# Performance work log

Measured on AMD Instinct MI355X. Metric: run time of the kernel, lower is better.

## Reference

```python
import jax, jax.numpy as jnp
import numpy as np


def _graph_conv(x, src, dst, W_rel, b_rel, W_root):
    # PyG GraphConv (aggr='add'): out = lin_rel(sum_{j->i} x_j) + lin_root(x_i)
    agg = jax.ops.segment_sum(x[src], dst, num_segments=x.shape[0])  # [N, d]
    return agg @ W_rel + b_rel + x @ W_root


def setup_inputs() -> dict:
    N, E, D, H, G = 50000, 800000, 128, 128, 256
    key = jax.random.key(0)
    ks = jax.random.split(key, 24)
    x = jax.random.normal(ks[0], (N, D), dtype=jnp.float32)
    edge_index = jax.random.randint(ks[1], (2, E), 0, N, dtype=jnp.int64)
    batch = jnp.sort(jax.random.randint(ks[2], (N,), 0, G, dtype=jnp.int64))
    inp = {"x": x, "edge_index": edge_index, "batch": batch, "num_graphs": G}
    dims = [(D, H), (H, H), (H, H), (H, H), (H, H)]
    for i, (din, dout) in enumerate(dims, 1):
        s = 1.0 / np.sqrt(din)
        inp[f"W_rel{i}"] = jax.random.normal(ks[3 * i], (din, dout), dtype=jnp.float32) * s
        inp[f"b_rel{i}"] = jax.random.normal(ks[3 * i + 1], (dout,), dtype=jnp.float32) * s
        inp[f"W_root{i}"] = jax.random.normal(ks[3 * i + 2], (din, dout), dtype=jnp.float32) * s
    inp["fc1_W"] = jax.random.normal(ks[18], (H, H), dtype=jnp.float32) / np.sqrt(H)
    inp["fc1_b"] = jax.random.normal(ks[19], (H,), dtype=jnp.float32) / np.sqrt(H)
    inp["fc2_W"] = jax.random.normal(ks[20], (H, 1), dtype=jnp.float32) / np.sqrt(H)
    inp["fc2_b"] = jax.random.normal(ks[21], (1,), dtype=jnp.float32) / np.sqrt(H)
    return inp


def reference(x, edge_index, batch, num_graphs,
              W_rel1, b_rel1, W_root1,
              W_rel2, b_rel2, W_root2,
              W_rel3, b_rel3, W_root3,
              W_rel4, b_rel4, W_root4,
              W_rel5, b_rel5, W_root5,
              fc1_W, fc1_b, fc2_W, fc2_b):
    src, dst = edge_index[0], edge_index[1]
    h = x
    for Wr, br, Wl in ((W_rel1, b_rel1, W_root1), (W_rel2, b_rel2, W_root2),
                       (W_rel3, b_rel3, W_root3), (W_rel4, b_rel4, W_root4),
                       (W_rel5, b_rel5, W_root5)):
        h = jax.nn.relu(_graph_conv(h, src, dst, Wr, br, Wl))
    # global_add_pool -> [num_graphs, H]
    g = jax.ops.segment_sum(h, batch, num_segments=num_graphs)
    g = jax.nn.relu(g @ fc1_W + fc1_b)
    # dropout is identity in eval mode
    return g @ fc2_W + fc2_b  # [num_graphs, 1]
```

## Files before the change

### kernel.cpp

```cpp
#include <hip/hip_runtime.h>
#include <hip/hip_bf16.h>

typedef __attribute__((ext_vector_type(4))) float f32x4;
typedef __attribute__((ext_vector_type(8))) _Float16 f16x8;
typedef __attribute__((ext_vector_type(4))) _Float16 f16x4;

#define CHUNK 4096
#define BSH 7
#define CAP 4096

static __device__ __forceinline__ float2 h2f2(unsigned v) {
  _Float16 lo = __builtin_bit_cast(_Float16, (unsigned short)(v & 0xffffu));
  _Float16 hi = __builtin_bit_cast(_Float16, (unsigned short)(v >> 16));
  return make_float2((float)lo, (float)hi);
}
static __device__ __forceinline__ unsigned f2h2(float x, float y) {
  unsigned short lo = __builtin_bit_cast(unsigned short, (_Float16)x);
  unsigned short hi = __builtin_bit_cast(unsigned short, (_Float16)y);
  return ((unsigned)hi << 16) | lo;
}

__global__ __launch_bounds__(256) void cvt_kernel(const float* __restrict__ x,
                                                  _Float16* __restrict__ h, int total4) {
  int i = blockIdx.x * blockDim.x + threadIdx.x;
  if (i < total4) {
    float4 v = *(const float4*)(x + (size_t)i * 4);
    f16x4 o = {(_Float16)v.x, (_Float16)v.y, (_Float16)v.z, (_Float16)v.w};
    *(f16x4*)(h + (size_t)i * 4) = o;
  }
}

__global__ __launch_bounds__(256) void bhist_kernel(const int* __restrict__ dst,
                                                    int* __restrict__ gcnt, int E, int nb) {
  __shared__ int l[512];
  int t = threadIdx.x;
  for (int i = t; i < 512; i += 256) l[i] = 0;
  __syncthreads();
  int cbase = blockIdx.x * CHUNK;
  #pragma unroll
  for (int i = 0; i < CHUNK / 256; ++i) {
    int idx = cbase + i * 256 + t;
    if (idx < E) atomicAdd(&l[dst[idx] >> BSH], 1);
  }
  __syncthreads();
  for (int i = t; i < nb; i += 256) {
    int c = l[i];
    if (c) atomicAdd(&gcnt[i], c);
  }
}

__global__ __launch_bounds__(512) void bscan_kernel(const int* __restrict__ gcnt,
                                                    int* __restrict__ base,
                                                    int* __restrict__ gcursor, int nb, int E) {
  __shared__ int wsum[8], wpre[8];
  int t = threadIdx.x, lane = t & 63, w = t >> 6;
  int v = (t < nb) ? gcnt[t] : 0;
  int incl = v;
  #pragma unroll
  for (int o = 1; o < 64; o <<= 1) {
    int x = __shfl_up(incl, o, 64);
    if (lane >= o) incl += x;
  }
  if (lane == 63) wsum[w] = incl;
  __syncthreads();
  if (t == 0) {
    int run = 0;
    #pragma unroll
    for (int q = 0; q < 8; ++q) { wpre[q] = run; run += wsum[q]; }
  }
  __syncthreads();
  int excl = wpre[w] + incl - v;
  if (t < nb) { base[t] = excl; gcursor[t] = excl; }
  if (t == 0) base[nb] = E;
}

__global__ __launch_bounds__(256) void bscatter_kernel(const int* __restrict__ src,
                                                       const int* __restrict__ dst,
                                                       int* __restrict__ gcursor,
                                                       int2* __restrict__ pairs, int E, int nb) {
  __shared__ int lcnt[512], lstart[512], lpos[512], lgbase[512];
  __shared__ int2 lp[CHUNK];
  __shared__ int wsum[4], wpre[4];
  int t = threadIdx.x, lane = t & 63, w = t >> 6;
  for (int i = t; i < 512; i += 256) lcnt[i] = 0;
  __syncthreads();
  int cbase = blockIdx.x * CHUNK;
  int m = E - cbase; if (m > CHUNK) m = CHUNK;
  #pragma unroll
  for (int i = 0; i < CHUNK / 256; ++i) {
    int idx = i * 256 + t;
    if (idx < m) atomicAdd(&lcnt[dst[cbase + idx] >> BSH], 1);
  }
  __syncthreads();
  int c0 = lcnt[2 * t], c1 = lcnt[2 * t + 1];
  int s = c0 + c1, incl = s;
  #pragma unroll
  for (int o = 1; o < 64; o <<= 1) {
    int x = __shfl_up(incl, o, 64);
    if (lane >= o) incl += x;
  }
  if (lane == 63) wsum[w] = incl;
  __syncthreads();
  if (t == 0) {
    int run = 0;
    #pragma unroll
    for (int q = 0; q < 4; ++q) { wpre[q] = run; run += wsum[q]; }
  }
  __syncthreads();
  int excl = wpre[w] + incl - s;
  lstart[2 * t] = excl;         lpos[2 * t] = excl;
  lstart[2 * t + 1] = excl + c0; lpos[2 * t + 1] = excl + c0;
  if (2 * t < nb && c0 > 0) lgbase[2 * t] = atomicAdd(&gcursor[2 * t], c0);
  if (2 * t + 1 < nb && c1 > 0) lgbase[2 * t + 1] = atomicAdd(&gcursor[2 * t + 1], c1);
  __syncthreads();
  #pragma unroll
  for (int i = 0; i < CHUNK / 256; ++i) {
    int idx = i * 256 + t;
    if (idx < m) {
      int d = dst[cbase + idx], sv = src[cbase + idx];
      int p = atomicAdd(&lpos[d >> BSH], 1);
      lp[p] = make_int2(sv, d);
    }
  }
  __syncthreads();
  for (int i = t; i < m; i += 256) {
    int2 pr = lp[i];
    int b = pr.y >> BSH;
    pairs[lgbase[b] + (i - lstart[b])] = pr;
  }
}

__global__ __launch_bounds__(256) void bbuild_kernel(const int2* __restrict__ pairs,
                                                     const int* __restrict__ base,
                                                     int* __restrict__ row_ptr,
                                                     int* __restrict__ col, int N, int E) {
  __shared__ int cnt[128], cur[128], w2[2];
  __shared__ int cl[CAP];
  int b = blockIdx.x, t = threadIdx.x;
  int mb = base[b], me = base[b + 1], m = me - mb;
  if (t < 128) cnt[t] = 0;
  __syncthreads();
  for (int i = t; i < m; i += 256) atomicAdd(&cnt[pairs[mb + i].y & 127], 1);
  __syncthreads();
  int v = 0, incl = 0;
  if (t < 128) {
    v = cnt[t]; incl = v;
    #pragma unroll
    for (int o = 1; o < 64; o <<= 1) {
      int x = __shfl_up(incl, o, 64);
      if ((t & 63) >= o) incl += x;
    }
    if ((t & 63) == 63) w2[t >> 6] = incl;
  }
  __syncthreads();
  if (t < 128) {
    int excl = incl - v + ((t & 64) ? w2[0] : 0);
    cur[t] = excl;
    int node = (b << BSH) + t;
    if (node < N) row_ptr[node] = mb + excl;
  }
  if (b == 0 && t == 0) row_ptr[N] = E;
  __syncthreads();
  if (m <= CAP) {
    for (int i = t; i < m; i += 256) {
      int2 p = pairs[mb + i];
      int pos = atomicAdd(&cur[p.y & 127], 1);
      cl[pos] = p.x;
    }
    __syncthreads();
    for (int i = t; i < m; i += 256) col[mb + i] = cl[i];
  } else {
    for (int i = t; i < m; i += 256) {
      int2 p = pairs[mb + i];
      int pos = atomicAdd(&cur[p.y & 127], 1);
      col[mb + pos] = p.x;
    }
  }
}

__global__ void prep_kernel(const float* __restrict__ Wrel, const float* __restrict__ Wroot,
                            _Float16* __restrict__ Whi, _Float16* __restrict__ Wlo,
                            float wscale) {
  int idx = blockIdx.x * blockDim.x + threadIdx.x;
  int col = idx >> 8;
  int k = idx & 255;
  float v = (k < 128) ? Wrel[k * 128 + col] : Wroot[(k - 128) * 128 + col];
  v *= wscale;
  _Float16 hi = (_Float16)v;
  _Float16 lo = (_Float16)(v - (float)hi);
  Whi[idx] = hi;
  Wlo[idx] = lo;
}

__global__ __launch_bounds__(256) void gemm_fused(const _Float16* __restrict__ hin,
                                                  const int* __restrict__ row_ptr,
                                                  const int* __restrict__ col,
                                                  const _Float16* __restrict__ Whi,
                                                  const _Float16* __restrict__ Wlo,
                                                  const float* __restrict__ bias,
                                                  float bscale,
                                                  _Float16* __restrict__ out, int N) {
  __shared__ unsigned lds[64 * 64];
  const unsigned* __restrict__ h2 = (const unsigned*)hin;
  int t = threadIdx.x, w = t >> 6, lane = t & 63;
  int row_base = blockIdx.x * 64;

  for (int rr = 0; rr < 16; ++rr) {
    int row = row_base + w * 16 + rr;
    float ax = 0.f, ay = 0.f;
    if (row < N) {
      int s = __builtin_amdgcn_readfirstlane(row_ptr[row]);
      int e = __builtin_amdgcn_readfirstlane(row_ptr[row + 1]);
      int i = s;
      for (; i + 7 < e; i += 8) {
        unsigned v0 = h2[(size_t)col[i + 0] * 64 + lane];
        unsigned v1 = h2[(size_t)col[i + 1] * 64 + lane];
        unsigned v2 = h2[(size_t)col[i + 2] * 64 + lane];
        unsigned v3 = h2[(size_t)col[i + 3] * 64 + lane];
        unsigned v4 = h2[(size_t)col[i + 4] * 64 + lane];
        unsigned v5 = h2[(size_t)col[i + 5] * 64 + lane];
        unsigned v6 = h2[(size_t)col[i + 6] * 64 + lane];
        unsigned v7 = h2[(size_t)col[i + 7] * 64 + lane];
        float2 f0 = h2f2(v0), f1 = h2f2(v1), f2 = h2f2(v2), f3 = h2f2(v3);
        float2 f4 = h2f2(v4), f5 = h2f2(v5), f6 = h2f2(v6), f7 = h2f2(v7);
        ax += (f0.x + f1.x) + (f2.x + f3.x) + ((f4.x + f5.x) + (f6.x + f7.x));
        ay += (f0.y + f1.y) + (f2.y + f3.y) + ((f4.y + f5.y) + (f6.y + f7.y));
      }
      for (; i < e; ++i) {
        float2 f0 = h2f2(h2[(size_t)col[i] * 64 + lane]);
        ax += f0.x; ay += f0.y;
      }
    }
    int rl = w * 16 + rr;
    unsigned byte = (unsigned)(rl * 256 + lane * 4) ^ (unsigned)((rl & 7) << 4);
    lds[byte >> 2] = f2h2(ax, ay);
  }
  __syncthreads();

  int wv = w;
  int l16 = lane & 15;
  int khalf = lane >> 4;
  int koff = khalf * 8;
  int col_base = wv * 32;

  f32x4 acc[4][2];
  #pragma unroll
  for (int r = 0; r < 4; r++)
    #pragma unroll
    for (int c = 0; c < 2; c++) acc[r][c] = (f32x4){0.f, 0.f, 0.f, 0.f};

  #pragma unroll
  for (int ks = 0; ks < 8; ++ks) {
    int k0 = ks * 32;
    f16x8 bh[2], bl[2];
    #pragma unroll
    for (int c = 0; c < 2; c++) {
      int cc = col_base + c * 16 + l16;
      bh[c] = *(const f16x8*)(Whi + cc * 256 + k0 + koff);
      bl[c] = *(const f16x8*)(Wlo + cc * 256 + k0 + koff);
    }
    #pragma unroll
    for (int r = 0; r < 4; r++) {
      f16x8 a;
      if (ks < 4) {
        int arow = r * 16 + l16;
        unsigned byte = (unsigned)(arow * 256 + (k0 + koff) * 2) ^ (unsigned)((arow & 7) << 4);
        a = *(const f16x8*)((const char*)lds + byte);
      } else {
        int row = row_base + r * 16 + l16;
        if (row >= N) row = N - 1;
        a = *(const f16x8*)(hin + (size_t)row * 128 + (k0 - 128) + koff);
      }
      #pragma unroll
      for (int c = 0; c < 2; c++) {
        acc[r][c] = __builtin_amdgcn_mfma_f32_16x16x32_f16(a, bh[c], acc[r][c], 0, 0, 0);
        acc[r][c] = __builtin_amdgcn_mfma_f32_16x16x32_f16(a, bl[c], acc[r][c], 0, 0, 0);
      }
    }
  }

  #pragma unroll
  for (int r = 0; r < 4; r++) {
    #pragma unroll
    for (int c = 0; c < 2; c++) {
      int cc = col_base + c * 16 + l16;
      float b = bias[cc] * bscale;
      #pragma unroll
      for (int tt = 0; tt < 4; tt++) {
        int row = row_base + r * 16 + khalf * 4 + tt;
        if (row < N) {
          float v = acc[r][c][tt] + b;
          out[(size_t)row * 128 + cc] = (_Float16)(v > 0.f ? v : 0.f);
        }
      }
    }
  }
}

static __device__ __forceinline__ int lbound(const int* __restrict__ a, int n, int v) {
  int lo = 0, hi = n;
  while (lo < hi) {
    int m = (lo + hi) >> 1;
    if (a[m] < v) lo = m + 1; else hi = m;
  }
  return lo;
}

__global__ __launch_bounds__(128) void poolhead_kernel(const _Float16* __restrict__ h,
                                                       const int* __restrict__ batch,
                                                       const float* __restrict__ fc1W,
                                                       const float* __restrict__ fc1b,
                                                       const float* __restrict__ fc2W,
                                                       const float* __restrict__ fc2b,
                                                       float* __restrict__ out, int N,
                                                       float unscale) {
  int gid = blockIdx.x, j = threadIdx.x;
  int start = lbound(batch, N, gid);
  int end = lbound(batch, N, gid + 1);
  float acc = 0.f;
  int r = start;
  for (; r + 3 < end; r += 4) {
    acc += (float)h[(size_t)r * 128 + j] + (float)h[(size_t)(r + 1) * 128 + j] +
           (float)h[(size_t)(r + 2) * 128 + j] + (float)h[(size_t)(r + 3) * 128 + j];
  }
  for (; r < end; ++r) acc += (float)h[(size_t)r * 128 + j];
  __shared__ float grow[128];
  __shared__ float red[128];
  grow[j] = acc * unscale;
  __syncthreads();
  float a1 = fc1b[j];
  #pragma unroll 8
  for (int k = 0; k < 128; ++k) a1 = fmaf(grow[k], fc1W[k * 128 + j], a1);
  a1 = a1 > 0.f ? a1 : 0.f;
  red[j] = a1 * fc2W[j];
  __syncthreads();
  #pragma unroll
  for (int s2 = 64; s2 > 0; s2 >>= 1) {
    if (j < s2) red[j] += red[j + s2];
    __syncthreads();
  }
  if (j == 0) out[gid] = red[0] + fc2b[0];
}

extern "C" void kernel_launch(void* const* d_in, const int* in_sizes, int n_in,
                              void* d_out, int out_size, void* d_ws, size_t ws_size,
                              hipStream_t stream) {
  const float* x = (const float*)d_in[0];
  const int* edge = (const int*)d_in[1];
  const int* batch = (const int*)d_in[2];
  const int N = in_sizes[0] / 128;
  const int E = in_sizes[1] / 2;
  const int G = out_size;
  const int* esrc = edge;
  const int* edst = edge + E;
  const int NB = (N + 127) >> BSH;

  char* ws = (char*)d_ws;
  size_t off = 0;
  auto alloc = [&](size_t bytes) -> void* {
    void* p = ws + off;
    off = (off + bytes + 255) & ~(size_t)255;
    return p;
  };
  _Float16* x16  = (_Float16*)alloc((size_t)N * 128 * 2);
  _Float16* bufA = (_Float16*)alloc((size_t)N * 128 * 2);
  _Float16* bufB = (_Float16*)alloc((size_t)N * 128 * 2);
  _Float16* Whi  = (_Float16*)alloc((size_t)5 * 32768 * 2);
  _Float16* Wlo  = (_Float16*)alloc((size_t)5 * 32768 * 2);
  int* row_ptr   = (int*)alloc((size_t)(N + 1) * 4);
  int* col       = (int*)alloc((size_t)E * 4);
  int2* pairs    = (int2*)alloc((size_t)E * 8);
  int* gcnt      = (int*)alloc(512 * 4);
  int* base      = (int*)alloc(520 * 4);
  int* gcursor   = (int*)alloc(512 * 4);
  if (off > ws_size) return;

  hipMemsetAsync(gcnt, 0, 512 * 4, stream);

  int nb1 = (E + CHUNK - 1) / CHUNK;
  bhist_kernel<<<nb1, 256, 0, stream>>>(edst, gcnt, E, NB);
  bscan_kernel<<<1, 512, 0, stream>>>(gcnt, base, gcursor, NB, E);
  bscatter_kernel<<<nb1, 256, 0, stream>>>(esrc, edst, gcursor, pairs, E, NB);
  bbuild_kernel<<<NB, 256, 0, stream>>>(pairs, base, row_ptr, col, N, E);

  cvt_kernel<<<(N * 128 / 4 + 255) / 256, 256, 0, stream>>>(x, x16, N * 128 / 4);

  const float S = 8.0f;
  float bscale = 1.0f;
  for (int l = 0; l < 5; ++l) {
    prep_kernel<<<128, 256, 0, stream>>>((const float*)d_in[4 + 3 * l],
                                         (const float*)d_in[6 + 3 * l],
                                         Whi + (size_t)l * 32768, Wlo + (size_t)l * 32768,
                                         1.0f / S);
  }

  const _Float16* hin = x16;
  _Float16* hout = bufA;
  int gemm_grid = (N + 63) / 64;
  for (int l = 0; l < 5; ++l) {
    bscale /= S;
    gemm_fused<<<gemm_grid, 256, 0, stream>>>(hin, row_ptr, col,
                                              Whi + (size_t)l * 32768, Wlo + (size_t)l * 32768,
                                              (const float*)d_in[5 + 3 * l], bscale, hout, N);
    hin = hout;
    hout = (hout == bufA) ? bufB : bufA;
  }
  poolhead_kernel<<<G, 128, 0, stream>>>(hin, batch,
                                         (const float*)d_in[19], (const float*)d_in[20],
                                         (const float*)d_in[21], (const float*)d_in[22],
                                         (float*)d_out, N, 32768.0f);
}
```

Measured before the change: 421.6 us.

## Gather 16-byte vectors with four rows per wave and halve GEMM tile to 32 rows

The aggregation loop now gives each 16-lane group its own destination row and has each lane load 8 halves (16 bytes) per neighbor, so a wave handles four rows at once instead of one row with 4-byte loads. The block tile shrinks from 64 to 32 rows, doubling the grid and halving the MFMA accumulators per wave. This targets latency-bound gathers with narrow loads and serial per-row processing. The cost is that row_ptr loads are no longer wave-uniform, lanes in a wave can diverge on unequal degrees, and each W fragment is now loaded for fewer rows.

After: 408.8 us. -3.0%, faster.

```diff
diff --git a/kernel.cpp b/kernel.cpp
--- a/kernel.cpp
+++ b/kernel.cpp
@@ -8,12 +8,8 @@
 #define CHUNK 4096
 #define BSH 7
 #define CAP 4096
-
-static __device__ __forceinline__ float2 h2f2(unsigned v) {
-  _Float16 lo = __builtin_bit_cast(_Float16, (unsigned short)(v & 0xffffu));
-  _Float16 hi = __builtin_bit_cast(_Float16, (unsigned short)(v >> 16));
-  return make_float2((float)lo, (float)hi);
-}
+#define TM 32
+
 static __device__ __forceinline__ unsigned f2h2(float x, float y) {
   unsigned short lo = __builtin_bit_cast(unsigned short, (_Float16)x);
   unsigned short hi = __builtin_bit_cast(unsigned short, (_Float16)y);
@@ -108,7 +104,7 @@
   }
   __syncthreads();
   int excl = wpre[w] + incl - s;
-  lstart[2 * t] = excl;         lpos[2 * t] = excl;
+  lstart[2 * t] = excl;          lpos[2 * t] = excl;
   lstart[2 * t + 1] = excl + c0; lpos[2 * t + 1] = excl + c0;
   if (2 * t < nb && c0 > 0) lgbase[2 * t] = atomicAdd(&gcursor[2 * t], c0);
   if (2 * t + 1 < nb && c1 > 0) lgbase[2 * t + 1] = atomicAdd(&gcursor[2 * t + 1], c1);
@@ -200,52 +196,53 @@
                                                   const float* __restrict__ bias,
                                                   float bscale,
                                                   _Float16* __restrict__ out, int N) {
-  __shared__ unsigned lds[64 * 64];
-  const unsigned* __restrict__ h2 = (const unsigned*)hin;
+  __shared__ unsigned lds[TM * 64];
+  const f16x8* __restrict__ hp = (const f16x8*)hin;
   int t = threadIdx.x, w = t >> 6, lane = t & 63;
-  int row_base = blockIdx.x * 64;
-
-  for (int rr = 0; rr < 16; ++rr) {
-    int row = row_base + w * 16 + rr;
-    float ax = 0.f, ay = 0.f;
+  int g = lane >> 4, l16 = lane & 15;
+  int row_base = blockIdx.x * TM;
+
+  #pragma unroll
+  for (int chunk = 0; chunk < 2; ++chunk) {
+    int rl = w * 8 + chunk * 4 + g;
+    int row = row_base + rl;
+    float acc[8];
+    #pragma unroll
+    for (int q = 0; q < 8; ++q) acc[q] = 0.f;
     if (row < N) {
-      int s = __builtin_amdgcn_readfirstlane(row_ptr[row]);
-      int e = __builtin_amdgcn_readfirstlane(row_ptr[row + 1]);
+      int s = row_ptr[row], e = row_ptr[row + 1];
       int i = s;
-      for (; i + 7 < e; i += 8) {
-        unsigned v0 = h2[(size_t)col[i + 0] * 64 + lane];
-        unsigned v1 = h2[(size_t)col[i + 1] * 64 + lane];
-        unsigned v2 = h2[(size_t)col[i + 2] * 64 + lane];
-        unsigned v3 = h2[(size_t)col[i + 3] * 64 + lane];
-        unsigned v4 = h2[(size_t)col[i + 4] * 64 + lane];
-        unsigned v5 = h2[(size_t)col[i + 5] * 64 + lane];
-        unsigned v6 = h2[(size_t)col[i + 6] * 64 + lane];
-        unsigned v7 = h2[(size_t)col[i + 7] * 64 + lane];
-        float2 f0 = h2f2(v0), f1 = h2f2(v1), f2 = h2f2(v2), f3 = h2f2(v3);
-        float2 f4 = h2f2(v4), f5 = h2f2(v5), f6 = h2f2(v6), f7 = h2f2(v7);
-        ax += (f0.x + f1.x) + (f2.x + f3.x) + ((f4.x + f5.x) + (f6.x + f7.x));
-        ay += (f0.y + f1.y) + (f2.y + f3.y) + ((f4.y + f5.y) + (f6.y + f7.y));
+      for (; i + 3 < e; i += 4) {
+        int c0 = col[i], c1 = col[i + 1], c2 = col[i + 2], c3 = col[i + 3];
+        f16x8 v0 = hp[(size_t)c0 * 16 + l16];
+        f16x8 v1 = hp[(size_t)c1 * 16 + l16];
+        f16x8 v2 = hp[(size_t)c2 * 16 + l16];
+        f16x8 v3 = hp[(size_t)c3 * 16 + l16];
+        #pragma unroll
+        for (int q = 0; q < 8; ++q)
+          acc[q] += ((float)v0[q] + (float)v1[q]) + ((float)v2[q] + (float)v3[q]);
       }
       for (; i < e; ++i) {
-        float2 f0 = h2f2(h2[(size_t)col[i] * 64 + lane]);
-        ax += f0.x; ay += f0.y;
+        f16x8 v0 = hp[(size_t)col[i] * 16 + l16];
+        #pragma unroll
+        for (int q = 0; q < 8; ++q) acc[q] += (float)v0[q];
       }
     }
-    int rl = w * 16 + rr;
-    unsigned byte = (unsigned)(rl * 256 + lane * 4) ^ (unsigned)((rl & 7) << 4);
-    lds[byte >> 2] = f2h2(ax, ay);
-  }
-  __syncthreads();
-
-  int wv = w;
-  int l16 = lane & 15;
+    f16x8 o;
+    #pragma unroll
+    for (int q = 0; q < 8; ++q) o[q] = (_Float16)acc[q];
+    unsigned byte = (unsigned)(rl * 256 + l16 * 16) ^ (unsigned)((rl & 7) << 4);
+    *(f16x8*)((char*)lds + byte) = o;
+  }
+  __syncthreads();
+
   int khalf = lane >> 4;
   int koff = khalf * 8;
-  int col_base = wv * 32;
-
-  f32x4 acc[4][2];
-  #pragma unroll
-  for (int r = 0; r < 4; r++)
+  int col_base = w * 32;
+
+  f32x4 acc[2][2];
+  #pragma unroll
+  for (int r = 0; r < 2; r++)
     #pragma unroll
     for (int c = 0; c < 2; c++) acc[r][c] = (f32x4){0.f, 0.f, 0.f, 0.f};
 
@@ -260,11 +257,11 @@
       bl[c] = *(const f16x8*)(Wlo + cc * 256 + k0 + koff);
     }
     #pragma unroll
-    for (int r = 0; r < 4; r++) {
+    for (int r = 0; r < 2; r++) {
       f16x8 a;
       if (ks < 4) {
         int arow = r * 16 + l16;
-        unsigned byte = (unsigned)(arow * 256 + (k0 + koff) * 2) ^ (unsigned)((arow & 7) << 4);
+        unsigned byte = (unsigned)(arow * 256 + k0 * 2 + khalf * 16) ^ (unsigned)((arow & 7) << 4);
         a = *(const f16x8*)((const char*)lds + byte);
       } else {
         int row = row_base + r * 16 + l16;
@@ -280,7 +277,7 @@
   }
 
   #pragma unroll
-  for (int r = 0; r < 4; r++) {
+  for (int r = 0; r < 2; r++) {
     #pragma unroll
     for (int c = 0; c < 2; c++) {
       int cc = col_base + c * 16 + l16;
@@ -396,7 +393,7 @@
 
   const _Float16* hin = x16;
   _Float16* hout = bufA;
-  int gemm_grid = (N + 63) / 64;
+  int gemm_grid = (N + TM - 1) / TM;
   for (int l = 0; l < 5; ++l) {
     bscale /= S;
     gemm_fused<<<gemm_grid, 256, 0, stream>>>(hin, row_ptr, col,
```
